# Kernel tuning notes

Hardware: AMD Instinct MI355X
Metric: run time of the kernel (lower is better)

Reference implementation:

```python
import jax, jax.numpy as jnp
import numpy as np

N = 40000      # nodes
E = 640000     # edges (avg degree 16)
H = 128        # hidden_dim
D = 4          # propagation_depth
G = 1250       # graphs in batch
T = 32         # target_dim
AF, AV = 9, 64   # atom categorical features, vocab per feature
BF, BV = 3, 8    # bond categorical features, vocab per feature


def silu(x):
    return x * jax.nn.sigmoid(x)


def setup_inputs() -> dict:
    key = jax.random.key(0)
    ks = jax.random.split(key, 32)
    s = 1.0 / np.sqrt(H)

    def w(i, shp, scale):
        return (jax.random.normal(ks[i], shp, jnp.float32) * scale).astype(jnp.float32)

    inp = {}
    inp["atom_feat"] = jax.random.randint(ks[0], (N, AF), 0, AV)
    inp["bond_feat"] = jax.random.randint(ks[1], (E, BF), 0, BV)
    inp["edge_src"] = jax.random.randint(ks[2], (E,), 0, N)
    inp["edge_dst"] = jax.random.randint(ks[3], (E,), 0, N)
    inp["node2graph"] = jnp.sort(jax.random.randint(ks[4], (N,), 0, G))

    inp["atom_emb"] = w(5, (AF, AV, H), 0.1)
    inp["bond_emb"] = w(6, (BF, BV, H), 0.1)
    # message MLP: Linear(3H,H)+SiLU, Linear(H,H)+SiLU (last_activation=mid_activation)
    inp["msg_W1"] = w(7, (D, 3 * H, H), 1.0 / np.sqrt(3 * H))
    inp["msg_b1"] = jnp.zeros((D, H), jnp.float32)
    inp["msg_W2"] = w(8, (D, H, H), s)
    inp["msg_b2"] = jnp.zeros((D, H), jnp.float32)
    # soft edge gate: Linear(H,1) + sigmoid
    inp["gate_W"] = w(9, (D, H, 1), s)
    inp["gate_b"] = jnp.zeros((D, 1), jnp.float32)
    # update MLP: Linear(H,H)+SiLU, Linear(H,H) (last None)
    inp["upd_W1"] = w(10, (D, H, H), s)
    inp["upd_b1"] = jnp.zeros((D, H), jnp.float32)
    inp["upd_W2"] = w(11, (D, H, H), s)
    inp["upd_b2"] = jnp.zeros((D, H), jnp.float32)
    # node_wise_output: Linear(H,H)+SiLU, Linear(H,H) (last None)
    inp["out_W1"] = w(12, (H, H), s)
    inp["out_b1"] = jnp.zeros((H,), jnp.float32)
    inp["out_W2"] = w(13, (H, H), s)
    inp["out_b2"] = jnp.zeros((H,), jnp.float32)
    # readout output MLP: Linear(3H,H)+ReLU, Linear(H,T) (last None)
    inp["ro_W1"] = w(14, (3 * H, H), 1.0 / np.sqrt(3 * H))
    inp["ro_b1"] = jnp.zeros((H,), jnp.float32)
    inp["ro_W2"] = w(15, (H, T), s)
    inp["ro_b2"] = jnp.zeros((T,), jnp.float32)
    return inp


def _forward(atom_feat, bond_feat, edge_src, edge_dst, node2graph,
             atom_emb, bond_emb,
             msg_W1, msg_b1, msg_W2, msg_b2, gate_W, gate_b,
             upd_W1, upd_b1, upd_W2, upd_b2,
             out_W1, out_b1, out_W2, out_b2,
             ro_W1, ro_b1, ro_W2, ro_b2):
    # Atom/Bond encoders: sum of per-feature categorical embeddings
    h = atom_emb[jnp.arange(AF), atom_feat].sum(axis=1)        # [N, H]
    e = bond_emb[jnp.arange(BF), bond_feat].sum(axis=1)        # [E, H]

    for l in range(D):
        src = h[edge_src]                                      # [E, H]
        dst = h[edge_dst]                                      # [E, H]
        m_in = jnp.concatenate([src, dst, e], axis=-1)         # [E, 3H]
        m = silu(silu(m_in @ msg_W1[l] + msg_b1[l]) @ msg_W2[l] + msg_b2[l])
        gate = jax.nn.sigmoid(m @ gate_W[l] + gate_b[l])       # [E, 1]
        m = m * gate
        m_sum = jax.ops.segment_sum(m, edge_dst, num_segments=N)  # [N, H]
        u_in = m_sum + h
        h_new = silu(u_in @ upd_W1[l] + upd_b1[l]) @ upd_W2[l] + upd_b2[l]
        h = h_new + h

    # node-wise output network
    h = silu(h @ out_W1 + out_b1) @ out_W2 + out_b2            # [N, H]

    # per-graph readouts: sum / mean / max
    sums = jax.ops.segment_sum(h, node2graph, num_segments=G)  # [G, H]
    cnt = jax.ops.segment_sum(jnp.ones((N, 1), h.dtype), node2graph, num_segments=G)
    mean = sums / jnp.maximum(cnt, 1.0)
    mx = jax.ops.segment_max(h, node2graph, num_segments=G)
    mx = jnp.where(cnt > 0, mx, 0.0)
    readout = jnp.concatenate([sums, mean, mx], axis=-1)       # [G, 3H]

    return jax.nn.relu(readout @ ro_W1 + ro_b1) @ ro_W2 + ro_b2  # [G, T]


def reference(atom_feat, bond_feat, edge_src, edge_dst, node2graph,
              atom_emb, bond_emb,
              msg_W1, msg_b1, msg_W2, msg_b2, gate_W, gate_b,
              upd_W1, upd_b1, upd_W2, upd_b2,
              out_W1, out_b1, out_W2, out_b2,
              ro_W1, ro_b1, ro_W2, ro_b2):
    return _forward(atom_feat, bond_feat, edge_src, edge_dst, node2graph,
                    atom_emb, bond_emb,
                    msg_W1, msg_b1, msg_W2, msg_b2, gate_W, gate_b,
                    upd_W1, upd_b1, upd_W2, upd_b2,
                    out_W1, out_b1, out_W2, out_b2,
                    ro_W1, ro_b1, ro_W2, ro_b2)
```

## Files before the change

kernel.cpp:

```cpp
#include <hip/hip_runtime.h>
#include <hip/hip_bf16.h>
#include <hip/hip_fp16.h>

#define NN 40000
#define NE 640000
#define HD 128
#define DEPTH 4
#define NG 1250
#define TD 32
#define AFN 9
#define AVN 64
#define BFN 3
#define BVN 8
#define NBLK (NE / 64)

typedef short bf16x8 __attribute__((ext_vector_type(8)));
typedef _Float16 f16x8 __attribute__((ext_vector_type(8)));
typedef _Float16 f16x2 __attribute__((ext_vector_type(2)));
typedef float f32x4 __attribute__((ext_vector_type(4)));

__device__ __forceinline__ uint cvtpk(float lo, float hi){
  uint r; asm("v_cvt_pk_bf16_f32 %0, %1, %2" : "=v"(r) : "v"(lo), "v"(hi)); return r;
}
__device__ __forceinline__ ushort f2bf(float x){ return (ushort)cvtpk(x, x); }
__device__ __forceinline__ float rcpfa(float x){ return __builtin_amdgcn_rcpf(x); }
__device__ __forceinline__ float siluf(float x){ return x * rcpfa(1.f + __expf(-x)); }
__device__ __forceinline__ float sigmf(float x){ return rcpfa(1.f + __expf(-x)); }
__device__ __forceinline__ uint packbf2(float a, float b){ return cvtpk(a, b); }

__device__ __forceinline__ __half2 silu_h2(__half2 x){
  const __half2 nl2e = __float2half2_rn(-1.44269504f);
  const __half2 one  = __float2half2_rn(1.f);
  __half2 e = h2exp2(__hmul2(x, nl2e));
  return __hmul2(x, h2rcp(__hadd2(one, e)));
}
union H2U { __half2 h; f16x2 v; uint u; };

__device__ __forceinline__ void pack_one(const float* __restrict__ src,
                                         ushort* __restrict__ dst,
                                         int K, int L, int isf16){
  int total = L * K * HD;
  for (int idx = blockIdx.x * blockDim.x + threadIdx.x; idx < total;
       idx += gridDim.x * blockDim.x){
    int l = idx / (K * HD);
    int r = idx - l * K * HD;
    int k = r / HD;
    int n = r - k * HD;
    float v = src[idx];
    ushort o;
    if (isf16){ __half hv = __float2half_rn(v); o = *(ushort*)&hv; }
    else o = f2bf(v);
    dst[(size_t)l * K * HD + ((size_t)(k >> 3) * HD + n) * 8 + (k & 7)] = o;
  }
}
__global__ void pack6(const float* s0, const float* s1, const float* s2,
                      const float* s3, const float* s4, const float* s5,
                      ushort* d0, ushort* d1, ushort* d2,
                      ushort* d3, ushort* d4, ushort* d5){
  switch (blockIdx.y){
    case 0: pack_one(s0, d0, 384, DEPTH, 0); break;
    case 1: pack_one(s1, d1, HD, DEPTH, 1); break;
    case 2: pack_one(s2, d2, HD, DEPTH, 0); break;
    case 3: pack_one(s3, d3, HD, DEPTH, 0); break;
    case 4: pack_one(s4, d4, HD, 1, 0); break;
    default: pack_one(s5, d5, HD, 1, 0); break;
  }
}

__global__ void zero_i(int* __restrict__ p, int n){
  for (int i = blockIdx.x * blockDim.x + threadIdx.x; i < n; i += gridDim.x * blockDim.x)
    p[i] = 0;
}

__global__ void atom_encode(const int* __restrict__ feat, const float* __restrict__ emb,
                            float* __restrict__ h, ushort* __restrict__ hbf){
  int n = blockIdx.x;
  int c = threadIdx.x;
  float acc = 0.f;
#pragma unroll
  for (int f = 0; f < AFN; ++f){
    int v = feat[n * AFN + f];
    acc += emb[(size_t)(f * AVN + v) * HD + c];
  }
  h[(size_t)n * HD + c] = acc;
  hbf[(size_t)n * HD + c] = f2bf(acc);
}

__global__ void ebf_k(const float* __restrict__ bemb, ushort* __restrict__ ebf){
  const int cid = blockIdx.x;
  const int c = threadIdx.x;
  const int f0 = cid >> 6, f1 = (cid >> 3) & 7, f2 = cid & 7;
  float v = bemb[(size_t)(0 * BVN + f0) * HD + c]
          + bemb[(size_t)(1 * BVN + f1) * HD + c]
          + bemb[(size_t)(2 * BVN + f2) * HD + c];
  ebf[(size_t)cid * HD + c] = f2bf(v);
}

__global__ void hist_k(const int* __restrict__ edst, int* __restrict__ deg){
  for (int e = blockIdx.x * blockDim.x + threadIdx.x; e < NE; e += gridDim.x * blockDim.x)
    atomicAdd(&deg[edst[e]], 1);
}

__global__ __launch_bounds__(1024) void scan_head(const int* __restrict__ deg,
                                                  int* __restrict__ head){
  __shared__ int buf[1024];
  const int t = threadIdx.x;
  const int base = t * 40;
  int s = 0;
  int dloc[40];
  if (t < 1000){
#pragma unroll
    for (int i = 0; i < 40; ++i){ dloc[i] = deg[base + i]; s += dloc[i]; }
  }
  buf[t] = s;
  __syncthreads();
  for (int ofs = 1; ofs < 1024; ofs <<= 1){
    int x = (t >= ofs) ? buf[t - ofs] : 0;
    __syncthreads();
    buf[t] += x;
    __syncthreads();
  }
  if (t < 1000){
    int run = buf[t] - s;
#pragma unroll
    for (int i = 0; i < 40; ++i){ head[base + i] = run; run += dloc[i]; }
  }
}

__global__ void scatter_k(const int* __restrict__ esrc, const int* __restrict__ edst,
                          const int* __restrict__ bfeat, int* __restrict__ head,
                          int* __restrict__ esrc_p, int* __restrict__ dst_p,
                          int* __restrict__ cid_p){
  for (int e = blockIdx.x * blockDim.x + threadIdx.x; e < NE; e += gridDim.x * blockDim.x){
    const int d = edst[e];
    const int pos = atomicAdd(&head[d], 1);
    esrc_p[pos] = esrc[e];
    dst_p[pos] = d;
    cid_p[pos] = bfeat[e * 3 + 0] * 64 + bfeat[e * 3 + 1] * 8 + bfeat[e * 3 + 2];
  }
}

__global__ __launch_bounds__(256) void pre_k(
    const ushort* __restrict__ hbf, const ushort* __restrict__ W1p,
    __half* __restrict__ prea, __half* __restrict__ preb,
    float* __restrict__ msum)
{
  const int tid = threadIdx.x;
  const int n0 = blockIdx.x * 64;
  {
    const float4 z = make_float4(0.f, 0.f, 0.f, 0.f);
    float4* mz = (float4*)(msum + (size_t)n0 * HD);
#pragma unroll
    for (int i = 0; i < 8; ++i) mz[tid + i * 256] = z;
  }
  const int lane = tid & 63, wv = tid >> 6;
  const int lr = lane & 15, lg = lane >> 4;
  const int arow = n0 + wv * 16 + lr;
  bf16x8 a[4];
#pragma unroll
  for (int ks = 0; ks < 4; ++ks)
    a[ks] = *(const bf16x8*)(hbf + (size_t)arow * HD + ks * 32 + lg * 8);
  const f32x4 zero = {0.f, 0.f, 0.f, 0.f};
  f32x4 acc[16];
#pragma unroll
  for (int i = 0; i < 16; ++i) acc[i] = zero;
#pragma unroll
  for (int ks = 0; ks < 4; ++ks){
#pragma unroll
    for (int ct = 0; ct < 16; ++ct){
      const int oct = ks * 4 + lg + ((ct >= 8) ? 16 : 0);
      const int ncol = (ct & 7) * 16 + lr;
      bf16x8 b = *(const bf16x8*)(W1p + ((size_t)oct * HD + ncol) * 8);
      acc[ct] = __builtin_amdgcn_mfma_f32_16x16x32_bf16(a[ks], b, acc[ct], 0, 0, 0);
    }
  }
#pragma unroll
  for (int ct = 0; ct < 16; ++ct){
    __half* dstp = (ct < 8) ? prea : preb;
    const int ncol = (ct & 7) * 16 + lr;
#pragma unroll
    for (int r = 0; r < 4; ++r){
      const int nrow = n0 + wv * 16 + lg * 4 + r;
      dstp[(size_t)nrow * HD + ncol] = __float2half_rn(acc[ct][r]);
    }
  }
}

__global__ __launch_bounds__(256) void ew1c_k(
    const ushort* __restrict__ ebf, const ushort* __restrict__ W1p_all,
    const float* __restrict__ b1_all, __half* __restrict__ ecb_all)
{
  const int l = blockIdx.y;
  const ushort* W1p = W1p_all + (size_t)l * 384 * HD;
  const float* b1v = b1_all + l * HD;
  __half* ecb = ecb_all + (size_t)l * 512 * HD;
  const int tid = threadIdx.x;
  const int c0 = blockIdx.x * 64;
  const int lane = tid & 63, wv = tid >> 6;
  const int lr = lane & 15, lg = lane >> 4;
  const int arow = c0 + wv * 16 + lr;
  bf16x8 a[4];
#pragma unroll
  for (int ks = 0; ks < 4; ++ks)
    a[ks] = *(const bf16x8*)(ebf + (size_t)arow * HD + ks * 32 + lg * 8);
  const f32x4 zero = {0.f, 0.f, 0.f, 0.f};
  f32x4 acc[8];
#pragma unroll
  for (int i = 0; i < 8; ++i) acc[i] = zero;
#pragma unroll
  for (int ks = 0; ks < 4; ++ks){
#pragma unroll
    for (int ct = 0; ct < 8; ++ct){
      const int oct = ks * 4 + lg + 32;
      const int ncol = ct * 16 + lr;
      bf16x8 b = *(const bf16x8*)(W1p + ((size_t)oct * HD + ncol) * 8);
      acc[ct] = __builtin_amdgcn_mfma_f32_16x16x32_bf16(a[ks], b, acc[ct], 0, 0, 0);
    }
  }
#pragma unroll
  for (int ct = 0; ct < 8; ++ct){
    const int ncol = ct * 16 + lr;
    const float bias = b1v[ncol];
#pragma unroll
    for (int r = 0; r < 4; ++r){
      const int nrow = c0 + wv * 16 + lg * 4 + r;
      ecb[(size_t)nrow * HD + ncol] = __float2half_rn(acc[ct][r] + bias);
    }
  }
}

__global__ __launch_bounds__(256, 6) void msg2_kernel(
    const __half* __restrict__ prea, const __half* __restrict__ preb,
    const __half* __restrict__ ecb,
    const int* __restrict__ esrc_p, const int* __restrict__ dst_p,
    const int* __restrict__ cid_p,
    const __half* __restrict__ W2p, const float* __restrict__ b2v,
    const float* __restrict__ gw, const float* __restrict__ gb,
    float* __restrict__ msum)
{
  __shared__ uint Ms[64 * 64];
  __shared__ int dsh[64];
  const int tid = threadIdx.x;
  const int bid = (int)blockIdx.x;
  const int bsw = (bid & 7) * (NBLK >> 3) + (bid >> 3);
  const int e0 = bsw * 64;
  if (tid < 64) dsh[tid] = dst_p[e0 + tid];

  const int lane = tid & 63;
  const int wv = tid >> 6;
  const int lr = lane & 15, lg = lane >> 4;
  const int row = e0 + wv * 16 + lr;
  const int s = esrc_p[row];
  const int d = dst_p[row];
  const int c = cid_p[row];

  f16x8 af[4];
#pragma unroll
  for (int ks = 0; ks < 4; ++ks){
    const int off = ks * 32 + lg * 8;
    union { uint4 q; __half2 h[4]; f16x8 v; } ua, ub, uc, uo;
    ua.q = *(const uint4*)(prea + (size_t)s * HD + off);
    ub.q = *(const uint4*)(preb + (size_t)d * HD + off);
    uc.q = *(const uint4*)(ecb + (size_t)c * HD + off);
#pragma unroll
    for (int j = 0; j < 4; ++j)
      uo.h[j] = silu_h2(__hadd2(__hadd2(ua.h[j], ub.h[j]), uc.h[j]));
    af[ks] = uo.v;
  }

  const f32x4 zero = {0.f, 0.f, 0.f, 0.f};
  f32x4 acc[8];
#pragma unroll
  for (int i = 0; i < 8; ++i) acc[i] = zero;
#pragma unroll
  for (int ks = 0; ks < 4; ++ks){
    const __half* wb = W2p + ((size_t)(ks * 4 + lg) * HD + lr) * 8;
#pragma unroll
    for (int ct = 0; ct < 8; ++ct){
      f16x8 b = *(const f16x8*)(wb + ct * 16 * 8);
      acc[ct] = __builtin_amdgcn_mfma_f32_16x16x32_f16(af[ks], b, acc[ct], 0, 0, 0);
    }
  }

  float b2l[4], b2h[4];
  __half2 gwh[4];
#pragma unroll
  for (int ct = 0; ct < 4; ++ct){
    b2l[ct] = b2v[ct * 16 + lr];
    b2h[ct] = b2v[ct * 16 + lr + 64];
    gwh[ct] = __floats2half2_rn(gw[ct * 16 + lr], gw[ct * 16 + lr + 64]);
  }
  __half2 mh[4][4];
#pragma unroll
  for (int ct = 0; ct < 4; ++ct){
#pragma unroll
    for (int r = 0; r < 4; ++r){
      __half2 x = __floats2half2_rn(acc[ct][r] + b2l[ct], acc[ct + 4][r] + b2h[ct]);
      mh[ct][r] = silu_h2(x);
    }
  }
  const float gbias = gb[0];
#pragma unroll
  for (int r = 0; r < 4; ++r){
    float sgs = 0.f;
#pragma unroll
    for (int ct = 0; ct < 4; ++ct){
      H2U a, b; a.h = mh[ct][r]; b.h = gwh[ct];
      sgs = __builtin_amdgcn_fdot2(a.v, b.v, sgs, false);
    }
    sgs += __shfl_xor(sgs, 1); sgs += __shfl_xor(sgs, 2);
    sgs += __shfl_xor(sgs, 4); sgs += __shfl_xor(sgs, 8);
    const __half2 gh = __float2half2_rn(sigmf(sgs + gbias));
#pragma unroll
    for (int ct = 0; ct < 4; ++ct) mh[ct][r] = __hmul2(mh[ct][r], gh);
  }

#pragma unroll
  for (int ct = 0; ct < 4; ++ct){
    const int ui = ct * 16 + lr;
#pragma unroll
    for (int r = 0; r < 4; ++r){
      const int lrow = wv * 16 + lg * 4 + r;
      H2U w; w.h = mh[ct][r];
      *(uint*)((char*)Ms + lrow * 256 + (((uint)(ui * 4)) ^ ((uint)((lrow & 7) << 4)))) = w.u;
    }
  }
  __syncthreads();

  {
    const int cp = tid & 63;
    const int seg = tid >> 6;
    const int r0 = seg * 16, r1 = r0 + 16;
    float rl = 0.f, rh = 0.f;
    int cur = dsh[r0];
    for (int r = r0; r < r1; ++r){
      const int dd = dsh[r];
      if (dd != cur){
        atomicAdd(&msum[(size_t)cur * HD + cp], rl);
        atomicAdd(&msum[(size_t)cur * HD + cp + 64], rh);
        rl = 0.f; rh = 0.f; cur = dd;
      }
      H2U w;
      w.u = *(const uint*)((const char*)Ms + r * 256 +
                           (((uint)(cp * 4)) ^ ((uint)((r & 7) << 4))));
      rl += __low2float(w.h); rh += __high2float(w.h);
    }
    atomicAdd(&msum[(size_t)cur * HD + cp], rl);
    atomicAdd(&msum[(size_t)cur * HD + cp + 64], rh);
  }
}

template <int MODE>
__global__ __launch_bounds__(256) void node_mlp(
    const float* hin, const float* __restrict__ msum,
    const ushort* __restrict__ W1p, const ushort* __restrict__ W2p,
    const float* __restrict__ b1v, const float* __restrict__ b2v,
    float* outp, ushort* __restrict__ hbf)
{
  __shared__ ushort At[64 * 128];
  __shared__ ushort Tt[64 * 128];
  const int tid = threadIdx.x;
  const int n0 = blockIdx.x * 64;

  {
    const int nl = tid >> 2, part = tid & 3;
    const int node = n0 + nl;
    const float4* hp = (const float4*)(hin + (size_t)node * HD + part * 32);
    const float4* mp = (MODE == 0) ? (const float4*)(msum + (size_t)node * HD + part * 32) : nullptr;
    char* rowp = (char*)At + nl * 256;
    const uint sw = (uint)((nl & 7) << 4);
#pragma unroll
    for (int j = 0; j < 4; ++j){
      float4 x0 = hp[j * 2 + 0], x1 = hp[j * 2 + 1];
      if (MODE == 0){
        float4 m0 = mp[j * 2 + 0], m1 = mp[j * 2 + 1];
        x0.x += m0.x; x0.y += m0.y; x0.z += m0.z; x0.w += m0.w;
        x1.x += m1.x; x1.y += m1.y; x1.z += m1.z; x1.w += m1.w;
      }
      uint4 o;
      o.x = packbf2(x0.x, x0.y); o.y = packbf2(x0.z, x0.w);
      o.z = packbf2(x1.x, x1.y); o.w = packbf2(x1.z, x1.w);
      uint cb = (uint)(part * 64 + j * 16);
      *(uint4*)(rowp + (cb ^ sw)) = o;
    }
  }
  __syncthreads();

  const int lane = tid & 63;
  const int wv = tid >> 6;
  const int lr = lane & 15, lg = lane >> 4;
  const int rowbase = wv * 16;
  const f32x4 zero = {0.f, 0.f, 0.f, 0.f};
  const int arow = rowbase + lr;
  const char* arp = (const char*)At + arow * 256;
  const uint asw = (uint)((arow & 7) << 4);

  f32x4 acc[8];
#pragma unroll
  for (int i = 0; i < 8; ++i) acc[i] = zero;
#pragma unroll
  for (int ks = 0; ks < 4; ++ks){
    uint cb = (uint)(ks * 64 + lg * 16);
    bf16x8 a = *(const bf16x8*)(arp + (cb ^ asw));
    const ushort* wbase = W1p + ((size_t)(ks * 4 + lg) * 128 + lr) * 8;
#pragma unroll
    for (int ct = 0; ct < 8; ++ct){
      bf16x8 b = *(const bf16x8*)(wbase + ct * 16 * 8);
      acc[ct] = __builtin_amdgcn_mfma_f32_16x16x32_bf16(a, b, acc[ct], 0, 0, 0);
    }
  }
#pragma unroll
  for (int ct = 0; ct < 8; ++ct){
    const int col = ct * 16 + lr;
    const float bias = b1v[col];
#pragma unroll
    for (int r = 0; r < 4; ++r){
      const int row = rowbase + lg * 4 + r;
      float v = siluf(acc[ct][r] + bias);
      *(ushort*)((char*)Tt + row * 256 + (((uint)(col * 2)) ^ ((uint)(row & 7) << 4))) = f2bf(v);
    }
  }
  __syncthreads();

  f32x4 acc2[8];
#pragma unroll
  for (int i = 0; i < 8; ++i) acc2[i] = zero;
  {
    const char* trp = (const char*)Tt + arow * 256;
#pragma unroll
    for (int ks = 0; ks < 4; ++ks){
      uint cb = (uint)(ks * 64 + lg * 16);
      bf16x8 a = *(const bf16x8*)(trp + (cb ^ asw));
      const ushort* wbase = W2p + ((size_t)(ks * 4 + lg) * 128 + lr) * 8;
#pragma unroll
      for (int ct = 0; ct < 8; ++ct){
        bf16x8 b = *(const bf16x8*)(wbase + ct * 16 * 8);
        acc2[ct] = __builtin_amdgcn_mfma_f32_16x16x32_bf16(a, b, acc2[ct], 0, 0, 0);
      }
    }
  }
#pragma unroll
  for (int ct = 0; ct < 8; ++ct){
    const int col = ct * 16 + lr;
    const float bias = b2v[col];
#pragma unroll
    for (int r = 0; r < 4; ++r){
      const int node = n0 + rowbase + lg * 4 + r;
      float v = acc2[ct][r] + bias;
      if (MODE == 0) v += hin[(size_t)node * HD + col];
      outp[(size_t)node * HD + col] = v;
      if (MODE == 0) hbf[(size_t)node * HD + col] = f2bf(v);
    }
  }
}

__global__ __launch_bounds__(128) void readout_final(
    const float* __restrict__ hout, const int* __restrict__ n2g,
    const float* __restrict__ W1, const float* __restrict__ b1,
    const float* __restrict__ W2, const float* __restrict__ b2,
    float* __restrict__ out){
  __shared__ float rsh[384];
  __shared__ float hr[128];
  const int g = blockIdx.x;
  const int c = threadIdx.x;
  int lo, hi;
  { int a = 0, b = NN; while (a < b){ int mid = (a + b) >> 1; if (n2g[mid] < g) a = mid + 1; else b = mid; } lo = a; }
  { int a = lo, b = NN; while (a < b){ int mid = (a + b) >> 1; if (n2g[mid] < g + 1) a = mid + 1; else b = mid; } hi = a; }
  float s = 0.f, mx = -3.4e38f;
  for (int n = lo; n < hi; ++n){
    float v = hout[(size_t)n * HD + c];
    s += v; mx = fmaxf(mx, v);
  }
  const int cnt = hi - lo;
  float mean = (cnt > 0) ? s / (float)cnt : 0.f;
  if (cnt == 0){ s = 0.f; mx = 0.f; }
  rsh[c] = s; rsh[128 + c] = mean; rsh[256 + c] = mx;
  __syncthreads();
  float acc = b1[c];
#pragma unroll 4
  for (int j = 0; j < 384; ++j) acc += rsh[j] * W1[j * 128 + c];
  hr[c] = fmaxf(acc, 0.f);
  __syncthreads();
  if (c < TD){
    float o = b2[c];
#pragma unroll 4
    for (int j = 0; j < 128; ++j) o += hr[j] * W2[j * TD + c];
    out[(size_t)g * TD + c] = o;
  }
}

extern "C" void kernel_launch(void* const* d_in, const int* in_sizes, int n_in,
                              void* d_out, int out_size, void* d_ws, size_t ws_size,
                              hipStream_t stream)
{
  const int*   atom_feat  = (const int*)  d_in[0];
  const int*   bond_feat  = (const int*)  d_in[1];
  const int*   edge_src   = (const int*)  d_in[2];
  const int*   edge_dst   = (const int*)  d_in[3];
  const int*   node2graph = (const int*)  d_in[4];
  const float* atom_emb   = (const float*)d_in[5];
  const float* bond_emb   = (const float*)d_in[6];
  const float* msg_W1     = (const float*)d_in[7];
  const float* msg_b1     = (const float*)d_in[8];
  const float* msg_W2     = (const float*)d_in[9];
  const float* msg_b2     = (const float*)d_in[10];
  const float* gate_W     = (const float*)d_in[11];
  const float* gate_b     = (const float*)d_in[12];
  const float* upd_W1     = (const float*)d_in[13];
  const float* upd_b1     = (const float*)d_in[14];
  const float* upd_W2     = (const float*)d_in[15];
  const float* upd_b2     = (const float*)d_in[16];
  const float* out_W1     = (const float*)d_in[17];
  const float* out_b1     = (const float*)d_in[18];
  const float* out_W2     = (const float*)d_in[19];
  const float* out_b2     = (const float*)d_in[20];
  const float* ro_W1      = (const float*)d_in[21];
  const float* ro_b1      = (const float*)d_in[22];
  const float* ro_W2      = (const float*)d_in[23];
  const float* ro_b2      = (const float*)d_in[24];
  (void)in_sizes; (void)n_in; (void)out_size; (void)ws_size;

  char* ws = (char*)d_ws;
  size_t off = 0;
  auto alloc = [&](size_t bytes) -> char* {
    char* p = ws + off;
    off = (off + bytes + 255) & ~(size_t)255;
    return p;
  };
  float*  h      = (float*) alloc((size_t)NN * HD * 4);
  ushort* hbf    = (ushort*)alloc((size_t)NN * HD * 2);
  float*  msum   = (float*) alloc((size_t)NN * HD * 4);
  ushort* msgW1p = (ushort*)alloc((size_t)DEPTH * 384 * HD * 2);
  ushort* msgW2p = (ushort*)alloc((size_t)DEPTH * HD * HD * 2);
  ushort* updW1p = (ushort*)alloc((size_t)DEPTH * HD * HD * 2);
  ushort* updW2p = (ushort*)alloc((size_t)DEPTH * HD * HD * 2);
  ushort* outW1p = (ushort*)alloc((size_t)HD * HD * 2);
  ushort* outW2p = (ushort*)alloc((size_t)HD * HD * 2);
  ushort* ebf    = (ushort*)alloc((size_t)512 * HD * 2);
  __half* ecb    = (__half*)alloc((size_t)DEPTH * 512 * HD * 2);
  __half* prea   = (__half*)alloc((size_t)NN * HD * 2);
  __half* preb   = (__half*)alloc((size_t)NN * HD * 2);
  int*    deg    = (int*)   alloc((size_t)NN * 4);
  int*    head   = (int*)   alloc((size_t)NN * 4);
  int*    esrc_p = (int*)   alloc((size_t)NE * 4);
  int*    dst_p  = (int*)   alloc((size_t)NE * 4);
  int*    cid_p  = (int*)   alloc((size_t)NE * 4);
  float*  hout   = msum;

  pack6<<<dim3(48, 6), 256, 0, stream>>>(msg_W1, msg_W2, upd_W1, upd_W2, out_W1, out_W2,
                                         msgW1p, msgW2p, updW1p, updW2p, outW1p, outW2p);
  atom_encode<<<NN, HD, 0, stream>>>(atom_feat, atom_emb, h, hbf);
  ebf_k<<<512, HD, 0, stream>>>(bond_emb, ebf);
  ew1c_k<<<dim3(8, DEPTH), 256, 0, stream>>>(ebf, msgW1p, msg_b1, ecb);

  zero_i<<<160, 256, 0, stream>>>(deg, NN);
  hist_k<<<640, 256, 0, stream>>>(edge_dst, deg);
  scan_head<<<1, 1024, 0, stream>>>(deg, head);
  scatter_k<<<640, 256, 0, stream>>>(edge_src, edge_dst, bond_feat, head,
                                     esrc_p, dst_p, cid_p);

  for (int l = 0; l < DEPTH; ++l){
    pre_k<<<NN / 64, 256, 0, stream>>>(hbf, msgW1p + (size_t)l * 384 * HD, prea, preb, msum);
    msg2_kernel<<<NBLK, 256, 0, stream>>>(
        prea, preb, ecb + (size_t)l * 512 * HD,
        esrc_p, dst_p, cid_p,
        (const __half*)msgW2p + (size_t)l * HD * HD,
        msg_b2 + l * HD, gate_W + l * HD, gate_b + l, msum);
    node_mlp<0><<<NN / 64, 256, 0, stream>>>(
        h, msum,
        updW1p + (size_t)l * HD * HD, updW2p + (size_t)l * HD * HD,
        upd_b1 + l * HD, upd_b2 + l * HD, h, hbf);
  }
  node_mlp<1><<<NN / 64, 256, 0, stream>>>(
      h, nullptr, outW1p, outW2p, out_b1, out_b2, hout, nullptr);
  readout_final<<<NG, 128, 0, stream>>>(hout, node2graph, ro_W1, ro_b1, ro_W2, ro_b2,
                                        (float*)d_out);
}
```

Baseline: 767.5 us.

## Process 128 edges per block in msg2 to reuse W2 fragments across two tiles

Each msg2 block now handles 128 edges instead of 64, and each wave computes two 16-row tiles that share the same W2 B-fragment loads. The segmented reduction then covers 32 rows per segment, which cuts the number of atomics at run boundaries. Float-to-half conversion in the epilogue now uses round-toward-zero pack instead of round-to-nearest. In exchange the kernel uses more registers and twice the LDS, and launch bounds drop from 6 to 4 blocks per CU, lowering occupancy.

Measured after the change: 710.6 us. 7.4% less time.

```diff
diff --git a/kernel.cpp b/kernel.cpp
--- a/kernel.cpp
+++ b/kernel.cpp
@@ -12,7 +12,7 @@
 #define AVN 64
 #define BFN 3
 #define BVN 8
-#define NBLK (NE / 64)
+#define NBLK2 (NE / 128)
 
 typedef short bf16x8 __attribute__((ext_vector_type(8)));
 typedef _Float16 f16x8 __attribute__((ext_vector_type(8)));
@@ -35,6 +35,10 @@
   return __hmul2(x, h2rcp(__hadd2(one, e)));
 }
 union H2U { __half2 h; f16x2 v; uint u; };
+__device__ __forceinline__ __half2 pkrtz(float lo, float hi){
+  auto t = __builtin_amdgcn_cvt_pkrtz(lo, hi);
+  H2U r; __builtin_memcpy(&r.u, &t, 4); return r.h;
+}
 
 __device__ __forceinline__ void pack_one(const float* __restrict__ src,
                                          ushort* __restrict__ dst,
@@ -229,7 +233,63 @@
   }
 }
 
-__global__ __launch_bounds__(256, 6) void msg2_kernel(
+__device__ __forceinline__ void build_af(
+    const __half* __restrict__ prea, const __half* __restrict__ preb,
+    const __half* __restrict__ ecb, int s, int d, int c, int lg, f16x8* af)
+{
+#pragma unroll
+  for (int ks = 0; ks < 4; ++ks){
+    const int off = ks * 32 + lg * 8;
+    union { uint4 q; __half2 h[4]; f16x8 v; } ua, ub, uc, uo;
+    ua.q = *(const uint4*)(prea + (size_t)s * HD + off);
+    ub.q = *(const uint4*)(preb + (size_t)d * HD + off);
+    uc.q = *(const uint4*)(ecb + (size_t)c * HD + off);
+#pragma unroll
+    for (int j = 0; j < 4; ++j)
+      uo.h[j] = silu_h2(__hadd2(__hadd2(ua.h[j], ub.h[j]), uc.h[j]));
+    af[ks] = uo.v;
+  }
+}
+
+__device__ __forceinline__ void edge_epilogue(
+    f32x4* acc, int lr, int lg, int rowbase,
+    const float* b2l, const float* b2h, const __half2* gwh, float gbias,
+    uint* Ms)
+{
+  __half2 mh[4][4];
+#pragma unroll
+  for (int ct = 0; ct < 4; ++ct){
+#pragma unroll
+    for (int r = 0; r < 4; ++r)
+      mh[ct][r] = silu_h2(pkrtz(acc[ct][r] + b2l[ct], acc[ct + 4][r] + b2h[ct]));
+  }
+#pragma unroll
+  for (int r = 0; r < 4; ++r){
+    float sgs = 0.f;
+#pragma unroll
+    for (int ct = 0; ct < 4; ++ct){
+      H2U a, b; a.h = mh[ct][r]; b.h = gwh[ct];
+      sgs = __builtin_amdgcn_fdot2(a.v, b.v, sgs, false);
+    }
+    sgs += __shfl_xor(sgs, 1); sgs += __shfl_xor(sgs, 2);
+    sgs += __shfl_xor(sgs, 4); sgs += __shfl_xor(sgs, 8);
+    const __half2 gh = __float2half2_rn(sigmf(sgs + gbias));
+#pragma unroll
+    for (int ct = 0; ct < 4; ++ct) mh[ct][r] = __hmul2(mh[ct][r], gh);
+  }
+#pragma unroll
+  for (int ct = 0; ct < 4; ++ct){
+    const int ui = ct * 16 + lr;
+#pragma unroll
+    for (int r = 0; r < 4; ++r){
+      const int lrow = rowbase + lg * 4 + r;
+      H2U w; w.h = mh[ct][r];
+      *(uint*)((char*)Ms + lrow * 256 + (((uint)(ui * 4)) ^ ((uint)((lrow & 7) << 4)))) = w.u;
+    }
+  }
+}
+
+__global__ __launch_bounds__(256, 4) void msg2_kernel(
     const __half* __restrict__ prea, const __half* __restrict__ preb,
     const __half* __restrict__ ecb,
     const int* __restrict__ esrc_p, const int* __restrict__ dst_p,
@@ -238,47 +298,38 @@
     const float* __restrict__ gw, const float* __restrict__ gb,
     float* __restrict__ msum)
 {
-  __shared__ uint Ms[64 * 64];
-  __shared__ int dsh[64];
+  __shared__ uint Ms[128 * 64];
+  __shared__ int dsh[128];
   const int tid = threadIdx.x;
   const int bid = (int)blockIdx.x;
-  const int bsw = (bid & 7) * (NBLK >> 3) + (bid >> 3);
-  const int e0 = bsw * 64;
-  if (tid < 64) dsh[tid] = dst_p[e0 + tid];
+  const int bsw = (bid & 7) * (NBLK2 >> 3) + (bid >> 3);
+  const int e0 = bsw * 128;
+  if (tid < 128) dsh[tid] = dst_p[e0 + tid];
 
   const int lane = tid & 63;
   const int wv = tid >> 6;
   const int lr = lane & 15, lg = lane >> 4;
-  const int row = e0 + wv * 16 + lr;
-  const int s = esrc_p[row];
-  const int d = dst_p[row];
-  const int c = cid_p[row];
-
-  f16x8 af[4];
-#pragma unroll
-  for (int ks = 0; ks < 4; ++ks){
-    const int off = ks * 32 + lg * 8;
-    union { uint4 q; __half2 h[4]; f16x8 v; } ua, ub, uc, uo;
-    ua.q = *(const uint4*)(prea + (size_t)s * HD + off);
-    ub.q = *(const uint4*)(preb + (size_t)d * HD + off);
-    uc.q = *(const uint4*)(ecb + (size_t)c * HD + off);
-#pragma unroll
-    for (int j = 0; j < 4; ++j)
-      uo.h[j] = silu_h2(__hadd2(__hadd2(ua.h[j], ub.h[j]), uc.h[j]));
-    af[ks] = uo.v;
-  }
+  const int row0 = e0 + wv * 16 + lr;
+  const int row1 = row0 + 64;
+  const int s0 = esrc_p[row0], d0 = dst_p[row0], c0 = cid_p[row0];
+  const int s1 = esrc_p[row1], d1 = dst_p[row1], c1 = cid_p[row1];
+
+  f16x8 af0[4], af1[4];
+  build_af(prea, preb, ecb, s0, d0, c0, lg, af0);
+  build_af(prea, preb, ecb, s1, d1, c1, lg, af1);
 
   const f32x4 zero = {0.f, 0.f, 0.f, 0.f};
-  f32x4 acc[8];
-#pragma unroll
-  for (int i = 0; i < 8; ++i) acc[i] = zero;
+  f32x4 acc0[8], acc1[8];
+#pragma unroll
+  for (int i = 0; i < 8; ++i){ acc0[i] = zero; acc1[i] = zero; }
 #pragma unroll
   for (int ks = 0; ks < 4; ++ks){
     const __half* wb = W2p + ((size_t)(ks * 4 + lg) * HD + lr) * 8;
 #pragma unroll
     for (int ct = 0; ct < 8; ++ct){
       f16x8 b = *(const f16x8*)(wb + ct * 16 * 8);
-      acc[ct] = __builtin_amdgcn_mfma_f32_16x16x32_f16(af[ks], b, acc[ct], 0, 0, 0);
+      acc0[ct] = __builtin_amdgcn_mfma_f32_16x16x32_f16(af0[ks], b, acc0[ct], 0, 0, 0);
+      acc1[ct] = __builtin_amdgcn_mfma_f32_16x16x32_f16(af1[ks], b, acc1[ct], 0, 0, 0);
     }
   }
 
@@ -288,49 +339,17 @@
   for (int ct = 0; ct < 4; ++ct){
     b2l[ct] = b2v[ct * 16 + lr];
     b2h[ct] = b2v[ct * 16 + lr + 64];
-    gwh[ct] = __floats2half2_rn(gw[ct * 16 + lr], gw[ct * 16 + lr + 64]);
-  }
-  __half2 mh[4][4];
-#pragma unroll
-  for (int ct = 0; ct < 4; ++ct){
-#pragma unroll
-    for (int r = 0; r < 4; ++r){
-      __half2 x = __floats2half2_rn(acc[ct][r] + b2l[ct], acc[ct + 4][r] + b2h[ct]);
-      mh[ct][r] = silu_h2(x);
-    }
+    gwh[ct] = pkrtz(gw[ct * 16 + lr], gw[ct * 16 + lr + 64]);
   }
   const float gbias = gb[0];
-#pragma unroll
-  for (int r = 0; r < 4; ++r){
-    float sgs = 0.f;
-#pragma unroll
-    for (int ct = 0; ct < 4; ++ct){
-      H2U a, b; a.h = mh[ct][r]; b.h = gwh[ct];
-      sgs = __builtin_amdgcn_fdot2(a.v, b.v, sgs, false);
-    }
-    sgs += __shfl_xor(sgs, 1); sgs += __shfl_xor(sgs, 2);
-    sgs += __shfl_xor(sgs, 4); sgs += __shfl_xor(sgs, 8);
-    const __half2 gh = __float2half2_rn(sigmf(sgs + gbias));
-#pragma unroll
-    for (int ct = 0; ct < 4; ++ct) mh[ct][r] = __hmul2(mh[ct][r], gh);
-  }
-
-#pragma unroll
-  for (int ct = 0; ct < 4; ++ct){
-    const int ui = ct * 16 + lr;
-#pragma unroll
-    for (int r = 0; r < 4; ++r){
-      const int lrow = wv * 16 + lg * 4 + r;
-      H2U w; w.h = mh[ct][r];
-      *(uint*)((char*)Ms + lrow * 256 + (((uint)(ui * 4)) ^ ((uint)((lrow & 7) << 4)))) = w.u;
-    }
-  }
+  edge_epilogue(acc0, lr, lg, wv * 16, b2l, b2h, gwh, gbias, Ms);
+  edge_epilogue(acc1, lr, lg, 64 + wv * 16, b2l, b2h, gwh, gbias, Ms);
   __syncthreads();
 
   {
     const int cp = tid & 63;
     const int seg = tid >> 6;
-    const int r0 = seg * 16, r1 = r0 + 16;
+    const int r0 = seg * 32, r1 = r0 + 32;
     float rl = 0.f, rh = 0.f;
     int cur = dsh[r0];
     for (int r = r0; r < r1; ++r){
@@ -561,7 +580,7 @@
 
   for (int l = 0; l < DEPTH; ++l){
     pre_k<<<NN / 64, 256, 0, stream>>>(hbf, msgW1p + (size_t)l * 384 * HD, prea, preb, msum);
-    msg2_kernel<<<NBLK, 256, 0, stream>>>(
+    msg2_kernel<<<NBLK2, 256, 0, stream>>>(
         prea, preb, ecb + (size_t)l * 512 * HD,
         esrc_p, dst_p, cid_p,
         (const __half*)msgW2p + (size_t)l * HD * HD,
```
